# Optimization experiments

Measured on AMD Instinct MI355X. Metric: run time of the kernel, lower is better.

Reference implementation:

```python
import jax, jax.numpy as jnp
import numpy as np

N, L, D = 32768, 15, 256
VOCAB, SCORE_MAX = 27, 100


def setup_inputs() -> dict:
    key = jax.random.key(0)
    ks = jax.random.split(key, 16)
    inp = {
        'words': jax.random.randint(ks[0], (N, L), 0, VOCAB, dtype=jnp.int32),
        'rows': jax.random.randint(ks[1], (N,), 0, L, dtype=jnp.int32),
        'cols': jax.random.randint(ks[2], (N,), 0, L, dtype=jnp.int32),
        'dirs': jax.random.randint(ks[3], (N,), 0, 2, dtype=jnp.int32),
        'scores': jax.random.randint(ks[4], (N,), 0, 150, dtype=jnp.int32),
        'letter_emb': jax.random.normal(ks[5], (VOCAB, D), jnp.float32),
        'positional': jax.random.normal(ks[6], (L, D), jnp.float32),
        'Wq': jax.random.normal(ks[7], (D, D), jnp.float32) / np.sqrt(D),
        'bq': jax.random.normal(ks[8], (D,), jnp.float32) * 0.01,
        'Wk': jax.random.normal(ks[9], (D, D), jnp.float32) / np.sqrt(D),
        'bk': jax.random.normal(ks[10], (D,), jnp.float32) * 0.01,
        'Wv': jax.random.normal(ks[11], (D, D), jnp.float32) / np.sqrt(D),
        'bv': jax.random.normal(ks[12], (D,), jnp.float32) * 0.01,
        'row_emb': jax.random.normal(ks[13], (L, D), jnp.float32),
        'col_emb': jax.random.normal(ks[14], (L, D), jnp.float32),
        'dir_emb': jax.random.normal(ks[15], (2, D), jnp.float32),
        'score_emb': jax.random.normal(jax.random.fold_in(key, 99), (SCORE_MAX, D), jnp.float32),
    }
    return inp


def reference(words, rows, cols, dirs, scores, letter_emb, positional, Wq, bq, Wk, bk, Wv, bv, row_emb, col_emb, dir_emb, score_emb):
    # WordEncoder: letter embedding + positional, then single-head self-attention, sum over positions
    emb = letter_emb[words] + positional[None, :, :]            # [N, L, D]
    q = emb @ Wq.T + bq                                          # [N, L, D]
    k = emb @ Wk.T + bk
    v = emb @ Wv.T + bv
    att = jax.nn.softmax(jnp.einsum('nld,nmd->nlm', q, k), axis=-1)  # [N, L, L]
    word = jnp.einsum('nlm,nmd->nd', att, v)                     # (att @ v).sum(axis=1) -> [N, D]
    # VectorEncoder
    vector = row_emb[rows] + col_emb[cols] + dir_emb[dirs]       # [N, D]
    # score embedding (clamped to score_max - 1)
    score_v = score_emb[jnp.minimum(scores, SCORE_MAX - 1)]      # [N, D]
    # original computes word_enc(move.word) twice (word + ordered) -> 2 * word
    return 2.0 * word + vector + score_v
```

## Files before the change

kernel.cpp:

```cpp
#include <hip/hip_runtime.h>
#include <hip/hip_bf16.h>

#define NMOV 32768
#define LW 15
#define DIM 256
#define NVOC 27
#define NR 405
#define GSH 408
#define MPB 8

__device__ __forceinline__ float b2f(unsigned short u) {
    return __uint_as_float(((unsigned int)u) << 16);
}

__device__ const unsigned char PAIR_LUT[120] = {
    0x00,
    0x10,0x11,
    0x20,0x21,0x22,
    0x30,0x31,0x32,0x33,
    0x40,0x41,0x42,0x43,0x44,
    0x50,0x51,0x52,0x53,0x54,0x55,
    0x60,0x61,0x62,0x63,0x64,0x65,0x66,
    0x70,0x71,0x72,0x73,0x74,0x75,0x76,0x77,
    0x80,0x81,0x82,0x83,0x84,0x85,0x86,0x87,0x88,
    0x90,0x91,0x92,0x93,0x94,0x95,0x96,0x97,0x98,0x99,
    0xA0,0xA1,0xA2,0xA3,0xA4,0xA5,0xA6,0xA7,0xA8,0xA9,0xAA,
    0xB0,0xB1,0xB2,0xB3,0xB4,0xB5,0xB6,0xB7,0xB8,0xB9,0xBA,0xBB,
    0xC0,0xC1,0xC2,0xC3,0xC4,0xC5,0xC6,0xC7,0xC8,0xC9,0xCA,0xCB,0xCC,
    0xD0,0xD1,0xD2,0xD3,0xD4,0xD5,0xD6,0xD7,0xD8,0xD9,0xDA,0xDB,0xDC,0xDD,
    0xE0,0xE1,0xE2,0xE3,0xE4,0xE5,0xE6,0xE7,0xE8,0xE9,0xEA,0xEB,0xEC,0xED,0xEE
};

__global__ __launch_bounds__(256) void qkv_gemm(
    const float* __restrict__ le, const float* __restrict__ pos,
    const float* __restrict__ Wq, const float* __restrict__ bq,
    const float* __restrict__ Wk, const float* __restrict__ bk,
    const float* __restrict__ Wv, const float* __restrict__ bv,
    float* __restrict__ QT, float* __restrict__ KT,
    __hip_bfloat16* __restrict__ VT)
{
    __shared__ float Ash[32][260];
    __shared__ float Bsh[256][69];
    const int t  = threadIdx.x;
    const int gx = blockIdx.x % 12;
    const int gy = blockIdx.x / 12;
    const int r0 = gy * 32;
    const int mat = gx >> 2;
    const int nb  = (gx & 3) * 64;
    const float* W  = (mat == 0) ? Wq : (mat == 1) ? Wk : Wv;
    const float* bb = (mat == 0) ? bq : (mat == 1) ? bk : bv;

    #pragma unroll
    for (int s = 0; s < 8; ++s) {
        int slot = s * 256 + t;
        int row = slot >> 6, q4 = slot & 63;
        int r = r0 + row;
        float4 v = make_float4(0.f, 0.f, 0.f, 0.f);
        if (r < NR) {
            int c = r / 15, l = r - c * 15;
            float4 lv = *(const float4*)&le[c * DIM + q4 * 4];
            float4 pv = *(const float4*)&pos[l * DIM + q4 * 4];
            v = make_float4(lv.x + pv.x, lv.y + pv.y, lv.z + pv.z, lv.w + pv.w);
        }
        *(float4*)&Ash[row][q4 * 4] = v;
    }
    #pragma unroll
    for (int s = 0; s < 16; ++s) {
        int slot = s * 256 + t;
        int row = slot >> 6, q4 = slot & 63;
        float4 w4 = *(const float4*)&W[(nb + row) * DIM + q4 * 4];
        Bsh[q4 * 4 + 0][row] = w4.x;
        Bsh[q4 * 4 + 1][row] = w4.y;
        Bsh[q4 * 4 + 2][row] = w4.z;
        Bsh[q4 * 4 + 3][row] = w4.w;
    }
    __syncthreads();

    const int tn = t & 63, tm = t >> 6;
    float acc[8];
    #pragma unroll
    for (int rr = 0; rr < 8; ++rr) acc[rr] = 0.f;

    #pragma unroll 4
    for (int kq = 0; kq < 64; ++kq) {
        float4 a4[8];
        #pragma unroll
        for (int rr = 0; rr < 8; ++rr)
            a4[rr] = *(const float4*)&Ash[tm * 8 + rr][kq * 4];
        float b0 = Bsh[kq * 4 + 0][tn];
        float b1 = Bsh[kq * 4 + 1][tn];
        float b2 = Bsh[kq * 4 + 2][tn];
        float b3 = Bsh[kq * 4 + 3][tn];
        #pragma unroll
        for (int rr = 0; rr < 8; ++rr)
            acc[rr] += a4[rr].x * b0 + a4[rr].y * b1 + a4[rr].z * b2 + a4[rr].w * b3;
    }

    const float bias = bb[nb + tn];
    const int dcol = nb + tn;
    #pragma unroll
    for (int rr = 0; rr < 8; ++rr) {
        int r = r0 + tm * 8 + rr;
        if (r < NR) {
            float v = acc[rr] + bias;
            if (mat == 0)      QT[r * DIM + dcol] = v;
            else if (mat == 1) KT[r * DIM + dcol] = v;
            else               VT[r * DIM + dcol] = __float2bfloat16(v);
        }
    }
}

__global__ __launch_bounds__(256) void h_matrix(
    const float* __restrict__ QT, const float* __restrict__ KT,
    float2* __restrict__ H)
{
    __shared__ float Qi[16][68], Ki[16][68], Qj[16][68], Kj[16][68];

    int rem = blockIdx.x, bi = 0, cnt = 26;
    while (rem >= cnt) { rem -= cnt; ++bi; --cnt; }
    const int bj = bi + rem;
    const int i0 = bi * 16, j0 = bj * 16;
    const int t = threadIdx.x;
    const int ti = t >> 4, tj = t & 15;

    float acc_ij = 0.f, acc_ji = 0.f;

    for (int k0 = 0; k0 < DIM; k0 += 64) {
        #pragma unroll
        for (int s = 0; s < 4; ++s) {
            int slot = s * 256 + t;
            int tile = slot >> 8;
            int r    = (slot >> 4) & 15;
            int c4   = slot & 15;
            int grow = (tile < 2) ? (i0 + r) : (j0 + r);
            const float* src = (tile == 0 || tile == 2) ? QT : KT;
            float4 v = (grow < NR)
                ? *(const float4*)&src[grow * DIM + k0 + c4 * 4]
                : make_float4(0.f, 0.f, 0.f, 0.f);
            float* dst = (tile == 0) ? &Qi[r][c4 * 4]
                       : (tile == 1) ? &Ki[r][c4 * 4]
                       : (tile == 2) ? &Qj[r][c4 * 4] : &Kj[r][c4 * 4];
            *(float4*)dst = v;
        }
        __syncthreads();
        #pragma unroll 4
        for (int k = 0; k < 64; k += 4) {
            float4 qi = *(const float4*)&Qi[ti][k];
            float4 kj = *(const float4*)&Kj[tj][k];
            float4 qj = *(const float4*)&Qj[ti][k];
            float4 ki = *(const float4*)&Ki[tj][k];
            acc_ij += qi.x * kj.x + qi.y * kj.y + qi.z * kj.z + qi.w * kj.w;
            acc_ji += qj.x * ki.x + qj.y * ki.y + qj.z * ki.z + qj.w * ki.w;
        }
        __syncthreads();
    }

    Qi[ti][tj] = acc_ij;
    Ki[ti][tj] = acc_ji;
    __syncthreads();
    const float t_ij = Qi[tj][ti];
    const float t_ji = Ki[tj][ti];

    const int i1 = i0 + ti, j1 = j0 + tj;
    if (i1 < NR && j1 < NR) H[i1 * GSH + j1] = make_float2(acc_ij, t_ji);
    const int i2 = j0 + ti, j2 = i0 + tj;
    if (i2 < NR && j2 < NR) H[i2 * GSH + j2] = make_float2(acc_ji, t_ij);
}

__global__ __launch_bounds__(256) void moves_kernel(
    const int* __restrict__ words, const int* __restrict__ rowsI,
    const int* __restrict__ colsI, const int* __restrict__ dirsI,
    const int* __restrict__ scoresI,
    const float2* __restrict__ H, const __hip_bfloat16* __restrict__ VT,
    const float* __restrict__ row_emb, const float* __restrict__ col_emb,
    const float* __restrict__ dir_emb, const float* __restrict__ score_emb,
    float* __restrict__ out)
{
    __shared__ float S[MPB][LW][17];
    __shared__ int   rIdx[MPB][16];
    __shared__ float csum[MPB][16];
    const int base = blockIdx.x * MPB;
    const int t = threadIdx.x;
    const int mv = t >> 5;
    const int j  = t & 31;

    if (j < LW)
        rIdx[mv][j] = words[(base + mv) * LW + j] * LW + j;
    __builtin_amdgcn_wave_barrier();

    const int wv = t >> 6;
    const int d0 = (t & 63) * 4;
    const unsigned short* VT16 = (const unsigned short*)VT;

    float2 hv[4];
    int ll[4], mm[4];
    #pragma unroll
    for (int k = 0; k < 4; ++k) {
        int p = j + 32 * k;
        if (p < 120) {
            int lm = PAIR_LUT[p];
            ll[k] = lm >> 4; mm[k] = lm & 15;
            int rl = rIdx[mv][ll[k]], rm = rIdx[mv][mm[k]];
            hv[k] = H[(size_t)rl * GSH + rm];
        }
    }

    const int iA = wv * 2, nA = base + iA;
    ushort4 vvA[LW];
    #pragma unroll
    for (int m = 0; m < LW; ++m) {
        int r = rIdx[iA][m];
        vvA[m] = *(const ushort4*)(VT16 + (size_t)r * DIM + d0);
    }
    float4 reA = *(const float4*)&row_emb[rowsI[nA] * DIM + d0];
    float4 ceA = *(const float4*)&col_emb[colsI[nA] * DIM + d0];
    float4 deA = *(const float4*)&dir_emb[dirsI[nA] * DIM + d0];
    float4 seA = *(const float4*)&score_emb[min(scoresI[nA], 99) * DIM + d0];

    #pragma unroll
    for (int k = 0; k < 4; ++k) {
        int p = j + 32 * k;
        if (p < 120) {
            S[mv][ll[k]][mm[k]] = hv[k].x;
            S[mv][mm[k]][ll[k]] = hv[k].y;
        }
    }
    __builtin_amdgcn_wave_barrier();

    if (j < LW) {
        float s[LW];
        #pragma unroll
        for (int m = 0; m < LW; ++m) s[m] = S[mv][j][m];
        float mx = s[0];
        #pragma unroll
        for (int m = 1; m < LW; ++m) mx = fmaxf(mx, s[m]);
        float sum = 0.f;
        #pragma unroll
        for (int m = 0; m < LW; ++m) { s[m] = __expf(s[m] - mx); sum += s[m]; }
        float inv = 1.0f / sum;
        #pragma unroll
        for (int m = 0; m < LW; ++m) S[mv][j][m] = s[m] * inv;
    }
    __builtin_amdgcn_wave_barrier();

    if (j < LW) {
        float acc = 0.f;
        #pragma unroll
        for (int l = 0; l < LW; ++l) acc += S[mv][l][j];
        csum[mv][j] = acc;
    }
    __builtin_amdgcn_wave_barrier();

    {
        float wx = 0.f, wy = 0.f, wz = 0.f, ww = 0.f;
        #pragma unroll
        for (int m = 0; m < LW; ++m) {
            float c = csum[iA][m];
            wx += c * b2f(vvA[m].x); wy += c * b2f(vvA[m].y);
            wz += c * b2f(vvA[m].z); ww += c * b2f(vvA[m].w);
        }
        float4 res;
        res.x = 2.f * wx + reA.x + ceA.x + deA.x + seA.x;
        res.y = 2.f * wy + reA.y + ceA.y + deA.y + seA.y;
        res.z = 2.f * wz + reA.z + ceA.z + deA.z + seA.z;
        res.w = 2.f * ww + reA.w + ceA.w + deA.w + seA.w;
        *(float4*)&out[(size_t)nA * DIM + d0] = res;
    }

    {
        const int iB = wv * 2 + 1, nB = base + iB;
        ushort4 vvB[LW];
        #pragma unroll
        for (int m = 0; m < LW; ++m) {
            int r = rIdx[iB][m];
            vvB[m] = *(const ushort4*)(VT16 + (size_t)r * DIM + d0);
        }
        float4 reB = *(const float4*)&row_emb[rowsI[nB] * DIM + d0];
        float4 ceB = *(const float4*)&col_emb[colsI[nB] * DIM + d0];
        float4 deB = *(const float4*)&dir_emb[dirsI[nB] * DIM + d0];
        float4 seB = *(const float4*)&score_emb[min(scoresI[nB], 99) * DIM + d0];

        float wx = 0.f, wy = 0.f, wz = 0.f, ww = 0.f;
        #pragma unroll
        for (int m = 0; m < LW; ++m) {
            float c = csum[iB][m];
            wx += c * b2f(vvB[m].x); wy += c * b2f(vvB[m].y);
            wz += c * b2f(vvB[m].z); ww += c * b2f(vvB[m].w);
        }
        float4 res;
        res.x = 2.f * wx + reB.x + ceB.x + deB.x + seB.x;
        res.y = 2.f * wy + reB.y + ceB.y + deB.y + seB.y;
        res.z = 2.f * wz + reB.z + ceB.z + deB.z + seB.z;
        res.w = 2.f * ww + reB.w + ceB.w + deB.w + seB.w;
        *(float4*)&out[(size_t)nB * DIM + d0] = res;
    }
}

extern "C" void kernel_launch(void* const* d_in, const int* in_sizes, int n_in,
                              void* d_out, int out_size, void* d_ws, size_t ws_size,
                              hipStream_t stream)
{
    const int*   words      = (const int*)d_in[0];
    const int*   rowsI      = (const int*)d_in[1];
    const int*   colsI      = (const int*)d_in[2];
    const int*   dirsI      = (const int*)d_in[3];
    const int*   scoresI    = (const int*)d_in[4];
    const float* letter_emb = (const float*)d_in[5];
    const float* positional = (const float*)d_in[6];
    const float* Wq         = (const float*)d_in[7];
    const float* bq         = (const float*)d_in[8];
    const float* Wk         = (const float*)d_in[9];
    const float* bk         = (const float*)d_in[10];
    const float* Wv         = (const float*)d_in[11];
    const float* bv         = (const float*)d_in[12];
    const float* row_emb    = (const float*)d_in[13];
    const float* col_emb    = (const float*)d_in[14];
    const float* dir_emb    = (const float*)d_in[15];
    const float* score_emb  = (const float*)d_in[16];
    float* out = (float*)d_out;

    float*  QT = (float*)d_ws;
    float*  KT = QT + NR * DIM;
    float2* Hm = (float2*)(KT + NR * DIM);
    __hip_bfloat16* VT = (__hip_bfloat16*)((char*)Hm + (size_t)NR * GSH * sizeof(float2));

    qkv_gemm<<<156, 256, 0, stream>>>(letter_emb, positional, Wq, bq, Wk, bk,
                                      Wv, bv, QT, KT, VT);
    h_matrix<<<351, 256, 0, stream>>>(QT, KT, Hm);
    moves_kernel<<<NMOV / MPB, 256, 0, stream>>>(words, rowsI, colsI, dirsI,
                                                 scoresI, Hm, VT, row_emb,
                                                 col_emb, dir_emb, score_emb,
                                                 out);
}
```

Baseline: 68.01 us.

## Process sixteen moves per block with two moves per half-wave and looped output

Doubles moves per block to sixteen. Each half-wave now gathers score pairs for two moves, and the softmax and column-sum stages pack four moves into the 60 active lanes of each wave. The output stage loops over four moves per wave, loading the V rows in two smaller batches, so the earlier prefetch of all V and embedding rows before the softmax is gone. This should raise lane utilisation and cut block count, at the cost of less load/compute overlap and a serialized output loop.

```diff
diff --git a/kernel.cpp b/kernel.cpp
--- a/kernel.cpp
+++ b/kernel.cpp
@@ -7,7 +7,7 @@
 #define NVOC 27
 #define NR 405
 #define GSH 408
-#define MPB 8
+#define MPB 16
 
 __device__ __forceinline__ float b2f(unsigned short u) {
     return __uint_as_float(((unsigned int)u) << 16);
@@ -180,19 +180,21 @@
     __shared__ int   rIdx[MPB][16];
     __shared__ float csum[MPB][16];
     const int base = blockIdx.x * MPB;
-    const int t = threadIdx.x;
-    const int mv = t >> 5;
+    const int t  = threadIdx.x;
+    const int w  = t >> 6;
+    const int ln = t & 63;
+    const int hw = t >> 5;
     const int j  = t & 31;
 
-    if (j < LW)
-        rIdx[mv][j] = words[(base + mv) * LW + j] * LW + j;
+    if (ln < 60) {
+        int mvl = ln / 15, row = ln - mvl * 15;
+        int mv = w * 4 + mvl;
+        rIdx[mv][row] = words[(base + mv) * LW + row] * LW + row;
+    }
     __builtin_amdgcn_wave_barrier();
 
-    const int wv = t >> 6;
-    const int d0 = (t & 63) * 4;
-    const unsigned short* VT16 = (const unsigned short*)VT;
-
-    float2 hv[4];
+    const int mv0 = hw * 2, mv1 = mv0 + 1;
+    float2 h0[4], h1[4];
     int ll[4], mm[4];
     #pragma unroll
     for (int k = 0; k < 4; ++k) {
@@ -200,37 +202,28 @@
         if (p < 120) {
             int lm = PAIR_LUT[p];
             ll[k] = lm >> 4; mm[k] = lm & 15;
-            int rl = rIdx[mv][ll[k]], rm = rIdx[mv][mm[k]];
-            hv[k] = H[(size_t)rl * GSH + rm];
-        }
-    }
-
-    const int iA = wv * 2, nA = base + iA;
-    ushort4 vvA[LW];
-    #pragma unroll
-    for (int m = 0; m < LW; ++m) {
-        int r = rIdx[iA][m];
-        vvA[m] = *(const ushort4*)(VT16 + (size_t)r * DIM + d0);
-    }
-    float4 reA = *(const float4*)&row_emb[rowsI[nA] * DIM + d0];
-    float4 ceA = *(const float4*)&col_emb[colsI[nA] * DIM + d0];
-    float4 deA = *(const float4*)&dir_emb[dirsI[nA] * DIM + d0];
-    float4 seA = *(const float4*)&score_emb[min(scoresI[nA], 99) * DIM + d0];
-
+            h0[k] = H[(size_t)rIdx[mv0][ll[k]] * GSH + rIdx[mv0][mm[k]]];
+            h1[k] = H[(size_t)rIdx[mv1][ll[k]] * GSH + rIdx[mv1][mm[k]]];
+        }
+    }
     #pragma unroll
     for (int k = 0; k < 4; ++k) {
         int p = j + 32 * k;
         if (p < 120) {
-            S[mv][ll[k]][mm[k]] = hv[k].x;
-            S[mv][mm[k]][ll[k]] = hv[k].y;
+            S[mv0][ll[k]][mm[k]] = h0[k].x;
+            S[mv0][mm[k]][ll[k]] = h0[k].y;
+            S[mv1][ll[k]][mm[k]] = h1[k].x;
+            S[mv1][mm[k]][ll[k]] = h1[k].y;
         }
     }
     __builtin_amdgcn_wave_barrier();
 
-    if (j < LW) {
+    if (ln < 60) {
+        int mvl = ln / 15, row = ln - mvl * 15;
+        int mv = w * 4 + mvl;
         float s[LW];
         #pragma unroll
-        for (int m = 0; m < LW; ++m) s[m] = S[mv][j][m];
+        for (int m = 0; m < LW; ++m) s[m] = S[mv][row][m];
         float mx = s[0];
         #pragma unroll
         for (int m = 1; m < LW; ++m) mx = fmaxf(mx, s[m]);
@@ -239,60 +232,57 @@
         for (int m = 0; m < LW; ++m) { s[m] = __expf(s[m] - mx); sum += s[m]; }
         float inv = 1.0f / sum;
         #pragma unroll
-        for (int m = 0; m < LW; ++m) S[mv][j][m] = s[m] * inv;
+        for (int m = 0; m < LW; ++m) S[mv][row][m] = s[m] * inv;
     }
     __builtin_amdgcn_wave_barrier();
 
-    if (j < LW) {
+    if (ln < 60) {
+        int mvl = ln / 15, col = ln - mvl * 15;
+        int mv = w * 4 + mvl;
         float acc = 0.f;
         #pragma unroll
-        for (int l = 0; l < LW; ++l) acc += S[mv][l][j];
-        csum[mv][j] = acc;
+        for (int l = 0; l < LW; ++l) acc += S[mv][l][col];
+        csum[mv][col] = acc;
     }
     __builtin_amdgcn_wave_barrier();
 
-    {
+    const int d0 = ln * 4;
+    const unsigned short* VT16 = (const unsigned short*)VT;
+    #pragma unroll 1
+    for (int s2 = 0; s2 < 4; ++s2) {
+        const int i = w * 4 + s2;
+        const int n = base + i;
+        float4 re = *(const float4*)&row_emb[rowsI[n] * DIM + d0];
+        float4 ce = *(const float4*)&col_emb[colsI[n] * DIM + d0];
+        float4 de = *(const float4*)&dir_emb[dirsI[n] * DIM + d0];
+        float4 se = *(const float4*)&score_emb[min(scoresI[n], 99) * DIM + d0];
+        ushort4 va[8];
+        #pragma unroll
+        for (int m = 0; m < 8; ++m)
+            va[m] = *(const ushort4*)(VT16 + (size_t)rIdx[i][m] * DIM + d0);
         float wx = 0.f, wy = 0.f, wz = 0.f, ww = 0.f;
         #pragma unroll
-        for (int m = 0; m < LW; ++m) {
-            float c = csum[iA][m];
-            wx += c * b2f(vvA[m].x); wy += c * b2f(vvA[m].y);
-            wz += c * b2f(vvA[m].z); ww += c * b2f(vvA[m].w);
+        for (int m = 0; m < 8; ++m) {
+            float c = csum[i][m];
+            wx += c * b2f(va[m].x); wy += c * b2f(va[m].y);
+            wz += c * b2f(va[m].z); ww += c * b2f(va[m].w);
+        }
+        ushort4 vb[7];
+        #pragma unroll
+        for (int m = 0; m < 7; ++m)
+            vb[m] = *(const ushort4*)(VT16 + (size_t)rIdx[i][8 + m] * DIM + d0);
+        #pragma unroll
+        for (int m = 0; m < 7; ++m) {
+            float c = csum[i][8 + m];
+            wx += c * b2f(vb[m].x); wy += c * b2f(vb[m].y);
+            wz += c * b2f(vb[m].z); ww += c * b2f(vb[m].w);
         }
         float4 res;
-        res.x = 2.f * wx + reA.x + ceA.x + deA.x + seA.x;
-        res.y = 2.f * wy + reA.y + ceA.y + deA.y + seA.y;
-        res.z = 2.f * wz + reA.z + ceA.z + deA.z + seA.z;
-        res.w = 2.f * ww + reA.w + ceA.w + deA.w + seA.w;
-        *(float4*)&out[(size_t)nA * DIM + d0] = res;
-    }
-
-    {
-        const int iB = wv * 2 + 1, nB = base + iB;
-        ushort4 vvB[LW];
-        #pragma unroll
-        for (int m = 0; m < LW; ++m) {
-            int r = rIdx[iB][m];
-            vvB[m] = *(const ushort4*)(VT16 + (size_t)r * DIM + d0);
-        }
-        float4 reB = *(const float4*)&row_emb[rowsI[nB] * DIM + d0];
-        float4 ceB = *(const float4*)&col_emb[colsI[nB] * DIM + d0];
-        float4 deB = *(const float4*)&dir_emb[dirsI[nB] * DIM + d0];
-        float4 seB = *(const float4*)&score_emb[min(scoresI[nB], 99) * DIM + d0];
-
-        float wx = 0.f, wy = 0.f, wz = 0.f, ww = 0.f;
-        #pragma unroll
-        for (int m = 0; m < LW; ++m) {
-            float c = csum[iB][m];
-            wx += c * b2f(vvB[m].x); wy += c * b2f(vvB[m].y);
-            wz += c * b2f(vvB[m].z); ww += c * b2f(vvB[m].w);
-        }
-        float4 res;
-        res.x = 2.f * wx + reB.x + ceB.x + deB.x + seB.x;
-        res.y = 2.f * wy + reB.y + ceB.y + deB.y + seB.y;
-        res.z = 2.f * wz + reB.z + ceB.z + deB.z + seB.z;
-        res.w = 2.f * ww + reB.w + ceB.w + deB.w + seB.w;
-        *(float4*)&out[(size_t)nB * DIM + d0] = res;
+        res.x = 2.f * wx + re.x + ce.x + de.x + se.x;
+        res.y = 2.f * wy + re.y + ce.y + de.y + se.y;
+        res.z = 2.f * wz + re.z + ce.z + de.z + se.z;
+        res.w = 2.f * ww + re.w + ce.w + de.w + se.w;
+        *(float4*)&out[(size_t)n * DIM + d0] = res;
     }
 }
 
```

Result: no change. 68.10 us (+0.1%).
